# Performance work log

Hardware: AMD Instinct MI355X
Metric: run time of the kernel (lower is better)

Reference implementation:

```python
import jax, jax.numpy as jnp
import numpy as np
import math

BATCH, NODES, IN_DIM = 8, 2048, 64
HEADS, OUT_DIM = 4, 32
D = HEADS * OUT_DIM
N_NEIGHBORS = 32


def setup_inputs() -> dict:
    key = jax.random.key(0)
    ks = jax.random.split(key, 6)
    s = lambda fan: 1.0 / np.sqrt(fan)
    return {
        "x": jax.random.normal(ks[0], (BATCH, NODES, IN_DIM), jnp.float32),
        "Wq": jax.random.normal(ks[1], (D, IN_DIM), jnp.float32) * s(IN_DIM),
        "bq": jnp.zeros((D,), jnp.float32),
        "Wk": jax.random.normal(ks[2], (D, IN_DIM), jnp.float32) * s(IN_DIM),
        "bk": jnp.zeros((D,), jnp.float32),
        "mlp_w": jax.random.normal(ks[3], (HEADS, HEADS), jnp.float32) * s(HEADS),
        "mlp_b": jnp.zeros((HEADS,), jnp.float32),
        "ln_g": jnp.ones((NODES,), jnp.float32),
        "ln_b": jnp.zeros((NODES,), jnp.float32),
    }


def _layernorm(x, g, b, eps=1e-5):
    m = x.mean(-1, keepdims=True)
    v = x.var(-1, keepdims=True)
    return (x - m) * jax.lax.rsqrt(v + eps) * g + b


def _forward(x, Wq, bq, Wk, bk, mlp_w, mlp_b, ln_g, ln_b):
    B, N, _ = x.shape
    # static graph branch (computed in the original forward, but its result is
    # never used in the returned adjacency -- kept for fidelity; DCE'd under jit)
    adj_static = jax.nn.softmax(
        jax.nn.relu(_layernorm(jnp.einsum('bnc,bmc->bnm', x, x), ln_g, ln_b)), axis=1)
    del adj_static

    q = x @ Wq.T + bq  # (B,N,D)
    k = x @ Wk.T + bk
    # (B,D,N) -> (B,H,d,N)
    q = q.transpose(0, 2, 1).reshape(B, HEADS, OUT_DIM, N)
    k = k.transpose(0, 2, 1).reshape(B, HEADS, OUT_DIM, N)
    q = q.transpose(0, 1, 3, 2)  # (B,H,N,d)

    # torch.split(query, chunk, dim=-1) splits q over out_dim, k over nodes; zip
    # truncates to the shorter list -> only min(nq,nk) chunks are processed.
    chunk = math.ceil(N / 2)
    nq = math.ceil(OUT_DIM / chunk)
    nk = math.ceil(N / chunk)
    inv_sqrt_d = jnp.float32(1.0 / math.sqrt(OUT_DIM))
    outs = []
    for i in range(min(nq, nk)):
        qc = q[..., i * chunk:(i + 1) * chunk]          # (B,H,N,dc)
        kc = k[..., i * chunk:(i + 1) * chunk]          # (B,H,d,Uc)
        a = jnp.einsum('bhnd,bhdu->bhnu', qc, kc) * inv_sqrt_d
        # dropout is identity in eval mode; soft-threshold with beta=0
        a = jnp.sign(a) * jax.nn.relu(jnp.abs(a))
        # 1x1 conv over head channels + relu, residual add
        a = jax.nn.relu(jnp.einsum('oh,bhnu->bonu', mlp_w, a)
                        + mlp_b[None, :, None, None]) + a
        outs.append(a)
    attn = jnp.concatenate(outs, axis=-1)               # (B,H,N,U)

    scores = attn.sum(axis=1)                           # (B,N,U)
    vals, idx = jax.lax.top_k(scores, N_NEIGHBORS)      # sorted, largest
    adj = jnp.zeros((B, N, N), x.dtype)
    bi = jnp.arange(B)[:, None, None]
    ni = jnp.arange(N)[None, :, None]
    return adj.at[bi, ni, idx].add(vals)


def reference(x, Wq, bq, Wk, bk, mlp_w, mlp_b, ln_g, ln_b):
    return _forward(x, Wq, bq, Wk, bk, mlp_w, mlp_b, ln_g, ln_b)
```

## Files before the change

### kernel.cpp

```cpp
#include <hip/hip_runtime.h>
#include <cstdint>
#include <cstddef>

#define BATCH 8
#define NODES 2048
#define IN_DIM 64
#define DTOT 128
#define NKEY 1024
#define QGROUPS 128
#define KGROUPS 64
#define SROW 1028

typedef _Float16 half8v __attribute__((ext_vector_type(8)));
typedef float float4v __attribute__((ext_vector_type(4)));

__device__ __forceinline__ unsigned long long make_key(float v, int idx) {
    unsigned u = __float_as_uint(v);
    u = (u & 0x80000000u) ? ~u : (u | 0x80000000u);
    return ((unsigned long long)u << 32) | (unsigned)(1023 - idx);
}

__device__ __forceinline__ float key_val(unsigned hi) {
    return __uint_as_float((hi & 0x80000000u) ? (hi & 0x7fffffffu) : ~hi);
}

__global__ __launch_bounds__(256) void proj_qk(
    const float* __restrict__ x, const float* __restrict__ Wq, const float* __restrict__ bq,
    const float* __restrict__ Wk, const float* __restrict__ bk,
    _Float16* __restrict__ qfh, _Float16* __restrict__ qfl,
    _Float16* __restrict__ kfh, _Float16* __restrict__ kfl)
{
    __shared__ float xs[64 * 68];
    __shared__ float wsh[64 * 68];

    const int t = threadIdx.x;
    const int blk = blockIdx.x;
    const int b = blk / 96;
    const int idx = blk - b * 96;

    const float* W; const float* bias;
    _Float16* oh; _Float16* ol;
    int nbase, cbase; size_t gbase;
    if (idx < 64) {
        int nt = idx >> 1, ct = idx & 1;
        nbase = nt * 64; cbase = ct * 64;
        W = Wq; bias = bq; oh = qfh; ol = qfl;
        gbase = (size_t)b * QGROUPS + (nbase >> 4);
    } else {
        int i2 = idx - 64;
        int nt = i2 >> 1, ct = i2 & 1;
        nbase = nt * 64; cbase = ct * 64;
        W = Wk; bias = bk; oh = kfh; ol = kfl;
        gbase = (size_t)b * KGROUPS + (nbase >> 4);
    }
    const int hbase = cbase >> 5;

    #pragma unroll
    for (int rep = 0; rep < 4; ++rep) {
        int f = rep * 256 + t;
        int r = f >> 4, d4 = f & 15;
        float4 xv = *(const float4*)(x + ((size_t)(b * NODES + nbase + r)) * IN_DIM + d4 * 4);
        *(float4*)(xs + r * 68 + d4 * 4) = xv;
        float4 wv = *(const float4*)(W + (size_t)(cbase + r) * IN_DIM + d4 * 4);
        *(float4*)(wsh + r * 68 + d4 * 4) = wv;
    }
    __syncthreads();

    const int w = t >> 6, l = t & 63;
    const int n_sel = w * 4 + (l >> 4);
    const int ul = l & 15;

    float acc[4][4];
    #pragma unroll
    for (int i = 0; i < 4; ++i)
        #pragma unroll
        for (int j = 0; j < 4; ++j) acc[i][j] = 0.f;

    #pragma unroll
    for (int d4 = 0; d4 < 16; ++d4) {
        float4 xv[4], wv[4];
        #pragma unroll
        for (int i = 0; i < 4; ++i)
            xv[i] = *(const float4*)(xs + (n_sel * 4 + i) * 68 + d4 * 4);
        #pragma unroll
        for (int j = 0; j < 4; ++j)
            wv[j] = *(const float4*)(wsh + (j * 16 + ul) * 68 + d4 * 4);
        #pragma unroll
        for (int i = 0; i < 4; ++i)
            #pragma unroll
            for (int j = 0; j < 4; ++j)
                acc[i][j] += xv[i].x * wv[j].x + xv[i].y * wv[j].y +
                             xv[i].z * wv[j].z + xv[i].w * wv[j].w;
    }
    __syncthreads();

    #pragma unroll
    for (int j = 0; j < 4; ++j) {
        float bv = bias[cbase + j * 16 + ul];
        #pragma unroll
        for (int i = 0; i < 4; ++i)
            xs[(n_sel * 4 + i) * 68 + j * 16 + ul] = acc[i][j] + bv;
    }
    __syncthreads();

    #pragma unroll
    for (int rep = 0; rep < 2; ++rep) {
        int u = rep * 256 + t;
        int g = u >> 7, hh = (u >> 6) & 1, lf = u & 63;
        const float* src = xs + (g * 16 + (lf & 15)) * 68 + hh * 32 + (lf >> 4) * 8;
        float4 f0 = *(const float4*)src;
        float4 f1 = *(const float4*)(src + 4);
        float tmp[8] = {f0.x, f0.y, f0.z, f0.w, f1.x, f1.y, f1.z, f1.w};
        half8v hv, lv;
        #pragma unroll
        for (int e = 0; e < 8; ++e) {
            _Float16 hi = (_Float16)tmp[e];
            hv[e] = hi;
            lv[e] = (_Float16)(tmp[e] - (float)hi);
        }
        size_t dst = ((gbase + g) * 4 + hbase + hh) * (size_t)512 + lf * 8;
        *(half8v*)(oh + dst) = hv;
        *(half8v*)(ol + dst) = lv;
    }
}

__global__ __launch_bounds__(512, 4) void scores_topk(
    const _Float16* __restrict__ qfh, const _Float16* __restrict__ qfl,
    const _Float16* __restrict__ kfh, const _Float16* __restrict__ kfl,
    const float* __restrict__ mlpw, const float* __restrict__ mlpb,
    float* __restrict__ adj)
{
    __shared__ float sc[16 * SROW];
    __shared__ unsigned long long cand[8][64];

    const int t = threadIdx.x;
    const int blk = blockIdx.x;
    const int b = blk & 7;
    const int gq = blk >> 3;

    const int w = t >> 6, l = t & 63;
    const int quad = l >> 4, lane16 = l & 15;

    half8v Ah[4], Al[4];
    #pragma unroll
    for (int h = 0; h < 4; ++h) {
        size_t a = (((size_t)b * QGROUPS + gq) * 4 + h) * 512 + l * 8;
        Ah[h] = *(const half8v*)(qfh + a);
        Al[h] = *(const half8v*)(qfl + a);
    }

    float mw[4][4], mb4[4];
    #pragma unroll
    for (int o = 0; o < 4; ++o) {
        mb4[o] = mlpb[o];
        #pragma unroll
        for (int h = 0; h < 4; ++h) mw[o][h] = mlpw[o * 4 + h];
    }
    const float INV = 0.17677669529663687f;

    #pragma unroll 2
    for (int i = 0; i < 8; ++i) {
        const int g = w * 8 + i;
        float4v C[4];
        #pragma unroll
        for (int h = 0; h < 4; ++h) {
            size_t a = (((size_t)b * KGROUPS + g) * 4 + h) * 512 + l * 8;
            half8v Bh = *(const half8v*)(kfh + a);
            half8v Bl = *(const half8v*)(kfl + a);
            float4v c = {0.f, 0.f, 0.f, 0.f};
            c = __builtin_amdgcn_mfma_f32_16x16x32_f16(Ah[h], Bh, c, 0, 0, 0);
            c = __builtin_amdgcn_mfma_f32_16x16x32_f16(Ah[h], Bl, c, 0, 0, 0);
            c = __builtin_amdgcn_mfma_f32_16x16x32_f16(Al[h], Bh, c, 0, 0, 0);
            C[h] = c;
        }
        #pragma unroll
        for (int r = 0; r < 4; ++r) {
            float a0 = C[0][r] * INV, a1 = C[1][r] * INV;
            float a2 = C[2][r] * INV, a3 = C[3][r] * INV;
            float ssum = a0 + a1 + a2 + a3;
            #pragma unroll
            for (int o = 0; o < 4; ++o) {
                float to = mw[o][0] * a0 + mw[o][1] * a1 + mw[o][2] * a2 + mw[o][3] * a3 + mb4[o];
                ssum += fmaxf(to, 0.f);
            }
            sc[(quad * 4 + r) * SROW + g * 16 + lane16] = ssum;
        }
    }
    __syncthreads();

    for (int rr = 0; rr < 2; ++rr) {
        const int row = w * 2 + rr;
        float* R = sc + row * SROW;

        float4 vv[4];
        #pragma unroll
        for (int jj = 0; jj < 4; ++jj) vv[jj] = *(const float4*)(R + jj * 256 + l * 4);

        float m = vv[0].x;
        #pragma unroll
        for (int jj = 0; jj < 4; ++jj) {
            m = fmaxf(m, vv[jj].x); m = fmaxf(m, vv[jj].y);
            m = fmaxf(m, vv[jj].z); m = fmaxf(m, vv[jj].w);
        }

        unsigned km;
        { unsigned s = __float_as_uint(m); km = (s & 0x80000000u) ? ~s : (s | 0x80000000u); }
        unsigned accT = 0u;
        #pragma unroll
        for (int bit = 31; bit >= 0; --bit) {
            unsigned trial = accT | (1u << bit);
            if (__popcll(__ballot(km >= trial)) >= 32) accT = trial;
        }
        const float T = key_val(accT);

        cand[w][l] = 0ull;
        __builtin_amdgcn_wave_barrier();
        int total = 0;
        #pragma unroll
        for (int jj = 0; jj < 4; ++jj) {
            #pragma unroll
            for (int e = 0; e < 4; ++e) {
                float v = (e == 0) ? vv[jj].x : (e == 1) ? vv[jj].y : (e == 2) ? vv[jj].z : vv[jj].w;
                bool p = (v >= T);
                unsigned long long msk = __ballot(p);
                if (p) {
                    int pos = total + __popcll(msk & ((1ull << l) - 1ull));
                    if (pos < 64) cand[w][pos] = make_key(v, jj * 256 + l * 4 + e);
                }
                total += (int)__popcll(msk);
            }
        }
        __builtin_amdgcn_wave_barrier();

        bool win = false; float wval = 0.f; int widx = 0;
        if (total <= 64) {
            unsigned long long key = cand[w][l];
            unsigned hi = (unsigned)(key >> 32), lo = (unsigned)key;

            unsigned X = 0u;
            #pragma unroll
            for (int bit = 31; bit >= 0; --bit) {
                unsigned trial = X | (1u << bit);
                if (__popcll(__ballot(hi >= trial)) >= 32) X = trial;
            }
            int cgt = __popcll(__ballot(hi > X));
            int rem = 32 - cgt;
            unsigned Y = 0u;
            #pragma unroll
            for (int bit = 9; bit >= 0; --bit) {
                unsigned trial = Y | (1u << bit);
                if (__popcll(__ballot(hi == X && lo >= trial)) >= rem) Y = trial;
            }
            if (hi > X || (hi == X && lo >= Y)) {
                win = true;
                wval = key_val(hi);
                widx = 1023 - (int)lo;
            }
        } else {
            float vals[16];
            #pragma unroll
            for (int jj = 0; jj < 4; ++jj) {
                vals[jj * 4 + 0] = vv[jj].x; vals[jj * 4 + 1] = vv[jj].y;
                vals[jj * 4 + 2] = vv[jj].z; vals[jj * 4 + 3] = vv[jj].w;
            }
            float selv = 0.f; int seli = 0;
            #pragma unroll 1
            for (int it = 0; it < 32; ++it) {
                float bv = -3.4e38f; int bi = 0x7fffffff;
                #pragma unroll
                for (int s = 0; s < 16; ++s) {
                    int idx2 = (s >> 2) * 256 + l * 4 + (s & 3);
                    if (vals[s] > bv) { bv = vals[s]; bi = idx2; }
                }
                #pragma unroll
                for (int off = 1; off < 64; off <<= 1) {
                    float ov = __shfl_xor(bv, off, 64);
                    int oi = __shfl_xor(bi, off, 64);
                    if (ov > bv || (ov == bv && oi < bi)) { bv = ov; bi = oi; }
                }
                if (l == it) { selv = bv; seli = bi; }
                if (((bi >> 2) & 63) == l) {
                    int slot = ((bi >> 8) << 2) + (bi & 3);
                    #pragma unroll
                    for (int s = 0; s < 16; ++s) if (s == slot) vals[s] = -3.4e38f;
                }
            }
            if (l < 32) { win = true; wval = selv; widx = seli; }
        }

        __builtin_amdgcn_wave_barrier();
        #pragma unroll
        for (int jj = 0; jj < 16; ++jj) R[l + (jj << 6)] = 0.f;
        __builtin_amdgcn_wave_barrier();
        if (win) R[widx] = wval;
        __builtin_amdgcn_wave_barrier();

        float* rowptr = adj + ((size_t)(b * NODES + gq * 16 + row)) * NODES;
        #pragma unroll
        for (int jj = 0; jj < 8; ++jj) {
            int c4 = jj * 64 + l;
            float4 val;
            if (c4 < 256) val = *(const float4*)(R + c4 * 4);
            else          val = make_float4(0.f, 0.f, 0.f, 0.f);
            *(float4*)(rowptr + c4 * 4) = val;
        }
    }
}

extern "C" void kernel_launch(void* const* d_in, const int* in_sizes, int n_in,
                              void* d_out, int out_size, void* d_ws, size_t ws_size,
                              hipStream_t stream) {
    const float* x    = (const float*)d_in[0];
    const float* Wq   = (const float*)d_in[1];
    const float* bq   = (const float*)d_in[2];
    const float* Wk   = (const float*)d_in[3];
    const float* bk   = (const float*)d_in[4];
    const float* mlpw = (const float*)d_in[5];
    const float* mlpb = (const float*)d_in[6];

    _Float16* qfh = (_Float16*)d_ws;
    _Float16* qfl = qfh + (size_t)BATCH * NODES * DTOT;
    _Float16* kfh = qfl + (size_t)BATCH * NODES * DTOT;
    _Float16* kfl = kfh + (size_t)BATCH * NKEY * DTOT;
    float* adj = (float*)d_out;

    proj_qk<<<dim3(BATCH * 96), dim3(256), 0, stream>>>(x, Wq, bq, Wk, bk, qfh, qfl, kfh, kfl);
    scores_topk<<<dim3(BATCH * QGROUPS), dim3(512), 0, stream>>>(qfh, qfl, kfh, kfl, mlpw, mlpb, adj);
}
```

Before: 186.1 us.

## Split score tile into two 512-column passes to halve LDS and raise occupancy

The score/top-k kernel now computes 512 key columns at a time into a half-size shared buffer. Each pass selects its own top 32 candidates and stores them as packed keys. A final merge picks the global top 32 from the 64 candidates and writes the output row in two halves. Halving shared memory per block lets the launch bounds ask for 6 blocks per CU instead of 4, aiming to hide latency better. The cost is an extra selection pass, an extra block barrier, and more register pressure under the tighter launch bound.

```diff
diff --git a/kernel.cpp b/kernel.cpp
--- a/kernel.cpp
+++ b/kernel.cpp
@@ -9,15 +9,18 @@
 #define NKEY 1024
 #define QGROUPS 128
 #define KGROUPS 64
-#define SROW 1028
+#define SROW2 516
 
 typedef _Float16 half8v __attribute__((ext_vector_type(8)));
 typedef float float4v __attribute__((ext_vector_type(4)));
 
+__device__ __forceinline__ unsigned key_hi_u(float v) {
+    unsigned u = __float_as_uint(v);
+    return (u & 0x80000000u) ? ~u : (u | 0x80000000u);
+}
+
 __device__ __forceinline__ unsigned long long make_key(float v, int idx) {
-    unsigned u = __float_as_uint(v);
-    u = (u & 0x80000000u) ? ~u : (u | 0x80000000u);
-    return ((unsigned long long)u << 32) | (unsigned)(1023 - idx);
+    return ((unsigned long long)key_hi_u(v) << 32) | (unsigned)(1023 - idx);
 }
 
 __device__ __forceinline__ float key_val(unsigned hi) {
@@ -124,14 +127,103 @@
     }
 }
 
-__global__ __launch_bounds__(512, 4) void scores_topk(
+__device__ __forceinline__ void select_pass32(
+    const float* R, int ubase, int l,
+    unsigned long long* candw, unsigned long long* keyrow)
+{
+    float4 vv0 = *(const float4*)(R + l * 4);
+    float4 vv1 = *(const float4*)(R + 256 + l * 4);
+    float elems[8] = {vv0.x, vv0.y, vv0.z, vv0.w, vv1.x, vv1.y, vv1.z, vv1.w};
+
+    float m = elems[0];
+    #pragma unroll
+    for (int s = 1; s < 8; ++s) m = fmaxf(m, elems[s]);
+
+    unsigned km = key_hi_u(m);
+    unsigned accT = 0u;
+    #pragma unroll
+    for (int bit = 31; bit >= 0; --bit) {
+        unsigned trial = accT | (1u << bit);
+        if (__popcll(__ballot(km >= trial)) >= 32) accT = trial;
+    }
+    const float T = key_val(accT);
+
+    candw[l] = 0ull;
+    __builtin_amdgcn_wave_barrier();
+    int total = 0;
+    #pragma unroll
+    for (int s = 0; s < 8; ++s) {
+        float v = elems[s];
+        bool p = (v >= T);
+        unsigned long long msk = __ballot(p);
+        if (p) {
+            int pos = total + __popcll(msk & ((1ull << l) - 1ull));
+            if (pos < 64) candw[pos] = make_key(v, ubase + (s >> 2) * 256 + l * 4 + (s & 3));
+        }
+        total += (int)__popcll(msk);
+    }
+    __builtin_amdgcn_wave_barrier();
+
+    if (total <= 64) {
+        unsigned long long key = candw[l];
+        unsigned hi = (unsigned)(key >> 32), lo = (unsigned)key;
+        unsigned X = 0u;
+        #pragma unroll
+        for (int bit = 31; bit >= 0; --bit) {
+            unsigned trial = X | (1u << bit);
+            if (__popcll(__ballot(hi >= trial)) >= 32) X = trial;
+        }
+        int cgt = __popcll(__ballot(hi > X));
+        int rem = 32 - cgt;
+        unsigned Y = 0u;
+        #pragma unroll
+        for (int bit = 9; bit >= 0; --bit) {
+            unsigned trial = Y | (1u << bit);
+            if (__popcll(__ballot(hi == X && lo >= trial)) >= rem) Y = trial;
+        }
+        bool win = (hi > X) || (hi == X && lo >= Y);
+        unsigned long long wm = __ballot(win);
+        if (win) keyrow[__popcll(wm & ((1ull << l) - 1ull))] = key;
+    } else {
+        float vals[8];
+        #pragma unroll
+        for (int s = 0; s < 8; ++s) vals[s] = elems[s];
+        float selv = 0.f; int seli = 0;
+        #pragma unroll 1
+        for (int it = 0; it < 32; ++it) {
+            float bv = -3.4e38f; int bi = 0x7fffffff;
+            #pragma unroll
+            for (int s = 0; s < 8; ++s) {
+                int lu = (s >> 2) * 256 + l * 4 + (s & 3);
+                if (vals[s] > bv) { bv = vals[s]; bi = lu; }
+            }
+            #pragma unroll
+            for (int off = 1; off < 64; off <<= 1) {
+                float ov = __shfl_xor(bv, off, 64);
+                int oi = __shfl_xor(bi, off, 64);
+                if (ov > bv || (ov == bv && oi < bi)) { bv = ov; bi = oi; }
+            }
+            if (l == it) { selv = bv; seli = bi; }
+            if (((bi >> 2) & 63) == l) {
+                int slot = ((bi >> 8) << 2) + (bi & 3);
+                #pragma unroll
+                for (int s = 0; s < 8; ++s) if (s == slot) vals[s] = -3.4e38f;
+            }
+        }
+        if (l < 32) keyrow[l] = make_key(selv, ubase + seli);
+    }
+    __builtin_amdgcn_wave_barrier();
+}
+
+__global__ __launch_bounds__(512, 6) void scores_topk(
     const _Float16* __restrict__ qfh, const _Float16* __restrict__ qfl,
     const _Float16* __restrict__ kfh, const _Float16* __restrict__ kfl,
     const float* __restrict__ mlpw, const float* __restrict__ mlpb,
     float* __restrict__ adj)
 {
-    __shared__ float sc[16 * SROW];
+    __shared__ float sc[16 * SROW2];
     __shared__ unsigned long long cand[8][64];
+    __shared__ unsigned long long keys[16][64];
 
     const int t = threadIdx.x;
     const int blk = blockIdx.x;
@@ -158,152 +250,95 @@
     }
     const float INV = 0.17677669529663687f;
 
-    #pragma unroll 2
-    for (int i = 0; i < 8; ++i) {
-        const int g = w * 8 + i;
-        float4v C[4];
-        #pragma unroll
-        for (int h = 0; h < 4; ++h) {
-            size_t a = (((size_t)b * KGROUPS + g) * 4 + h) * 512 + l * 8;
-            half8v Bh = *(const half8v*)(kfh + a);
-            half8v Bl = *(const half8v*)(kfl + a);
-            float4v c = {0.f, 0.f, 0.f, 0.f};
-            c = __builtin_amdgcn_mfma_f32_16x16x32_f16(Ah[h], Bh, c, 0, 0, 0);
-            c = __builtin_amdgcn_mfma_f32_16x16x32_f16(Ah[h], Bl, c, 0, 0, 0);
-            c = __builtin_amdgcn_mfma_f32_16x16x32_f16(Al[h], Bh, c, 0, 0, 0);
-            C[h] = c;
-        }
-        #pragma unroll
-        for (int r = 0; r < 4; ++r) {
-            float a0 = C[0][r] * INV, a1 = C[1][r] * INV;
-            float a2 = C[2][r] * INV, a3 = C[3][r] * INV;
-            float ssum = a0 + a1 + a2 + a3;
-            #pragma unroll
-            for (int o = 0; o < 4; ++o) {
-                float to = mw[o][0] * a0 + mw[o][1] * a1 + mw[o][2] * a2 + mw[o][3] * a3 + mb4[o];
-                ssum += fmaxf(to, 0.f);
-            }
-            sc[(quad * 4 + r) * SROW + g * 16 + lane16] = ssum;
-        }
-    }
-    __syncthreads();
+    #pragma unroll 1
+    for (int pass = 0; pass < 2; ++pass) {
+        #pragma unroll 2
+        for (int i = 0; i < 4; ++i) {
+            const int g = pass * 32 + w * 4 + i;
+            float4v C[4];
+            #pragma unroll
+            for (int h = 0; h < 4; ++h) {
+                size_t a = (((size_t)b * KGROUPS + g) * 4 + h) * 512 + l * 8;
+                half8v Bh = *(const half8v*)(kfh + a);
+                half8v Bl = *(const half8v*)(kfl + a);
+                float4v c = {0.f, 0.f, 0.f, 0.f};
+                c = __builtin_amdgcn_mfma_f32_16x16x32_f16(Ah[h], Bh, c, 0, 0, 0);
+                c = __builtin_amdgcn_mfma_f32_16x16x32_f16(Ah[h], Bl, c, 0, 0, 0);
+                c = __builtin_amdgcn_mfma_f32_16x16x32_f16(Al[h], Bh, c, 0, 0, 0);
+                C[h] = c;
+            }
+            #pragma unroll
+            for (int r = 0; r < 4; ++r) {
+                float a0 = C[0][r] * INV, a1 = C[1][r] * INV;
+                float a2 = C[2][r] * INV, a3 = C[3][r] * INV;
+                float ssum = a0 + a1 + a2 + a3;
+                #pragma unroll
+                for (int o = 0; o < 4; ++o) {
+                    float to = mw[o][0] * a0 + mw[o][1] * a1 + mw[o][2] * a2 + mw[o][3] * a3 + mb4[o];
+                    ssum += fmaxf(to, 0.f);
+                }
+                sc[(quad * 4 + r) * SROW2 + (w * 4 + i) * 16 + lane16] = ssum;
+            }
+        }
+        __syncthreads();
+
+        for (int rr = 0; rr < 2; ++rr) {
+            const int row = w * 2 + rr;
+            select_pass32(sc + row * SROW2, pass * 512, l, cand[w], &keys[row][pass * 32]);
+        }
+        if (pass == 0) __syncthreads();
+    }
 
     for (int rr = 0; rr < 2; ++rr) {
         const int row = w * 2 + rr;
-        float* R = sc + row * SROW;
-
-        float4 vv[4];
-        #pragma unroll
-        for (int jj = 0; jj < 4; ++jj) vv[jj] = *(const float4*)(R + jj * 256 + l * 4);
-
-        float m = vv[0].x;
-        #pragma unroll
-        for (int jj = 0; jj < 4; ++jj) {
-            m = fmaxf(m, vv[jj].x); m = fmaxf(m, vv[jj].y);
-            m = fmaxf(m, vv[jj].z); m = fmaxf(m, vv[jj].w);
-        }
-
-        unsigned km;
-        { unsigned s = __float_as_uint(m); km = (s & 0x80000000u) ? ~s : (s | 0x80000000u); }
-        unsigned accT = 0u;
+        unsigned long long key = keys[row][l];
+        unsigned hi = (unsigned)(key >> 32), lo = (unsigned)key;
+
+        unsigned X = 0u;
         #pragma unroll
         for (int bit = 31; bit >= 0; --bit) {
-            unsigned trial = accT | (1u << bit);
-            if (__popcll(__ballot(km >= trial)) >= 32) accT = trial;
-        }
-        const float T = key_val(accT);
-
-        cand[w][l] = 0ull;
-        __builtin_amdgcn_wave_barrier();
-        int total = 0;
-        #pragma unroll
-        for (int jj = 0; jj < 4; ++jj) {
-            #pragma unroll
-            for (int e = 0; e < 4; ++e) {
-                float v = (e == 0) ? vv[jj].x : (e == 1) ? vv[jj].y : (e == 2) ? vv[jj].z : vv[jj].w;
-                bool p = (v >= T);
-                unsigned long long msk = __ballot(p);
-                if (p) {
-                    int pos = total + __popcll(msk & ((1ull << l) - 1ull));
-                    if (pos < 64) cand[w][pos] = make_key(v, jj * 256 + l * 4 + e);
-                }
-                total += (int)__popcll(msk);
-            }
-        }
-        __builtin_amdgcn_wave_barrier();
-
-        bool win = false; float wval = 0.f; int widx = 0;
-        if (total <= 64) {
-            unsigned long long key = cand[w][l];
-            unsigned hi = (unsigned)(key >> 32), lo = (unsigned)key;
-
-            unsigned X = 0u;
-            #pragma unroll
-            for (int bit = 31; bit >= 0; --bit) {
-                unsigned trial = X | (1u << bit);
-                if (__popcll(__ballot(hi >= trial)) >= 32) X = trial;
-            }
-            int cgt = __popcll(__ballot(hi > X));
-            int rem = 32 - cgt;
-            unsigned Y = 0u;
-            #pragma unroll
-            for (int bit = 9; bit >= 0; --bit) {
-                unsigned trial = Y | (1u << bit);
-                if (__popcll(__ballot(hi == X && lo >= trial)) >= rem) Y = trial;
-            }
-            if (hi > X || (hi == X && lo >= Y)) {
-                win = true;
-                wval = key_val(hi);
-                widx = 1023 - (int)lo;
-            }
-        } else {
-            float vals[16];
-            #pragma unroll
-            for (int jj = 0; jj < 4; ++jj) {
-                vals[jj * 4 + 0] = vv[jj].x; vals[jj * 4 + 1] = vv[jj].y;
-                vals[jj * 4 + 2] = vv[jj].z; vals[jj * 4 + 3] = vv[jj].w;
-            }
-            float selv = 0.f; int seli = 0;
-            #pragma unroll 1
-            for (int it = 0; it < 32; ++it) {
-                float bv = -3.4e38f; int bi = 0x7fffffff;
-                #pragma unroll
-                for (int s = 0; s < 16; ++s) {
-                    int idx2 = (s >> 2) * 256 + l * 4 + (s & 3);
-                    if (vals[s] > bv) { bv = vals[s]; bi = idx2; }
-                }
-                #pragma unroll
-                for (int off = 1; off < 64; off <<= 1) {
-                    float ov = __shfl_xor(bv, off, 64);
-                    int oi = __shfl_xor(bi, off, 64);
-                    if (ov > bv || (ov == bv && oi < bi)) { bv = ov; bi = oi; }
-                }
-                if (l == it) { selv = bv; seli = bi; }
-                if (((bi >> 2) & 63) == l) {
-                    int slot = ((bi >> 8) << 2) + (bi & 3);
-                    #pragma unroll
-                    for (int s = 0; s < 16; ++s) if (s == slot) vals[s] = -3.4e38f;
-                }
-            }
-            if (l < 32) { win = true; wval = selv; widx = seli; }
-        }
-
-        __builtin_amdgcn_wave_barrier();
-        #pragma unroll
-        for (int jj = 0; jj < 16; ++jj) R[l + (jj << 6)] = 0.f;
-        __builtin_amdgcn_wave_barrier();
-        if (win) R[widx] = wval;
-        __builtin_amdgcn_wave_barrier();
-
+            unsigned trial = X | (1u << bit);
+            if (__popcll(__ballot(hi >= trial)) >= 32) X = trial;
+        }
+        int cgt = __popcll(__ballot(hi > X));
+        int rem = 32 - cgt;
+        unsigned Y = 0u;
+        #pragma unroll
+        for (int bit = 9; bit >= 0; --bit) {
+            unsigned trial = Y | (1u << bit);
+            if (__popcll(__ballot(hi == X && lo >= trial)) >= rem) Y = trial;
+        }
+        const bool win = (hi > X) || (hi == X && lo >= Y);
+        const float wval = key_val(hi);
+        const int widx = 1023 - (int)lo;
+
+        float* R = sc + row * SROW2;
         float* rowptr = adj + ((size_t)(b * NODES + gq * 16 + row)) * NODES;
-        #pragma unroll
-        for (int jj = 0; jj < 8; ++jj) {
-            int c4 = jj * 64 + l;
-            float4 val;
-            if (c4 < 256) val = *(const float4*)(R + c4 * 4);
-            else          val = make_float4(0.f, 0.f, 0.f, 0.f);
-            *(float4*)(rowptr + c4 * 4) = val;
-        }
+        const float4 z4 = make_float4(0.f, 0.f, 0.f, 0.f);
+
+        __builtin_amdgcn_wave_barrier();
+        *(float4*)(R + l * 4) = z4;
+        *(float4*)(R + 256 + l * 4) = z4;
+        __builtin_amdgcn_wave_barrier();
+        if (win && widx < 512) R[widx] = wval;
+        __builtin_amdgcn_wave_barrier();
+        #pragma unroll
+        for (int jj = 0; jj < 2; ++jj)
+            *(float4*)(rowptr + jj * 256 + l * 4) = *(const float4*)(R + jj * 256 + l * 4);
+
+        __builtin_amdgcn_wave_barrier();
+        *(float4*)(R + l * 4) = z4;
+        *(float4*)(R + 256 + l * 4) = z4;
+        __builtin_amdgcn_wave_barrier();
+        if (win && widx >= 512) R[widx - 512] = wval;
+        __builtin_amdgcn_wave_barrier();
+        #pragma unroll
+        for (int jj = 0; jj < 2; ++jj)
+            *(float4*)(rowptr + 512 + jj * 256 + l * 4) = *(const float4*)(R + jj * 256 + l * 4);
+
+        #pragma unroll
+        for (int jj = 0; jj < 4; ++jj)
+            *(float4*)(rowptr + 1024 + jj * 256 + l * 4) = z4;
     }
 }
 
```

New measurement: 218.9 us. 17.6% more time.

## Split top-k selection from dense adjacency write into separate kernel

Applied to the files above, without the earlier changes.

The scores kernel now writes only the 32 selected values and indices per row to a workspace. A new lightweight kernel scatters them into a shared-memory row and streams the full 2048-wide dense adjacency row, zeros included, to global memory. The aim is to decouple the large output write, roughly 134 MB, from the compute-heavy scoring kernel so the write runs at full bandwidth with high occupancy. It adds an extra launch and a small round trip through global memory for the selected entries.

```diff
diff --git a/kernel.cpp b/kernel.cpp
--- a/kernel.cpp
+++ b/kernel.cpp
@@ -124,11 +124,11 @@
     }
 }
 
-__global__ __launch_bounds__(512, 4) void scores_topk(
+__global__ __launch_bounds__(512, 4) void scores_sel(
     const _Float16* __restrict__ qfh, const _Float16* __restrict__ qfl,
     const _Float16* __restrict__ kfh, const _Float16* __restrict__ kfl,
     const float* __restrict__ mlpw, const float* __restrict__ mlpb,
-    float* __restrict__ adj)
+    float* __restrict__ kval, int* __restrict__ kidx)
 {
     __shared__ float sc[16 * SROW];
     __shared__ unsigned long long cand[8][64];
@@ -190,7 +190,8 @@
 
     for (int rr = 0; rr < 2; ++rr) {
         const int row = w * 2 + rr;
-        float* R = sc + row * SROW;
+        const float* R = sc + row * SROW;
+        const size_t grow = (size_t)(b * NODES + gq * 16 + row);
 
         float4 vv[4];
         #pragma unroll
@@ -232,7 +233,6 @@
         }
         __builtin_amdgcn_wave_barrier();
 
-        bool win = false; float wval = 0.f; int widx = 0;
         if (total <= 64) {
             unsigned long long key = cand[w][l];
             unsigned hi = (unsigned)(key >> 32), lo = (unsigned)key;
@@ -251,10 +251,12 @@
                 unsigned trial = Y | (1u << bit);
                 if (__popcll(__ballot(hi == X && lo >= trial)) >= rem) Y = trial;
             }
-            if (hi > X || (hi == X && lo >= Y)) {
-                win = true;
-                wval = key_val(hi);
-                widx = 1023 - (int)lo;
+            const bool win = (hi > X) || (hi == X && lo >= Y);
+            unsigned long long wm = __ballot(win);
+            if (win) {
+                int pos = __popcll(wm & ((1ull << l) - 1ull));
+                kval[grow * 32 + pos] = key_val(hi);
+                kidx[grow * 32 + pos] = 1023 - (int)lo;
             }
         } else {
             float vals[16];
@@ -285,25 +287,41 @@
                     for (int s = 0; s < 16; ++s) if (s == slot) vals[s] = -3.4e38f;
                 }
             }
-            if (l < 32) { win = true; wval = selv; widx = seli; }
-        }
-
-        __builtin_amdgcn_wave_barrier();
-        #pragma unroll
-        for (int jj = 0; jj < 16; ++jj) R[l + (jj << 6)] = 0.f;
-        __builtin_amdgcn_wave_barrier();
-        if (win) R[widx] = wval;
-        __builtin_amdgcn_wave_barrier();
-
-        float* rowptr = adj + ((size_t)(b * NODES + gq * 16 + row)) * NODES;
-        #pragma unroll
-        for (int jj = 0; jj < 8; ++jj) {
-            int c4 = jj * 64 + l;
-            float4 val;
-            if (c4 < 256) val = *(const float4*)(R + c4 * 4);
-            else          val = make_float4(0.f, 0.f, 0.f, 0.f);
-            *(float4*)(rowptr + c4 * 4) = val;
-        }
+            if (l < 32) {
+                kval[grow * 32 + l] = selv;
+                kidx[grow * 32 + l] = seli;
+            }
+        }
+    }
+}
+
+__global__ __launch_bounds__(256) void write_adj(
+    const float* __restrict__ kval, const int* __restrict__ kidx,
+    float* __restrict__ adj)
+{
+    __shared__ float rowbuf[2 * 1024];
+
+    const int t = threadIdx.x;
+    const int row0 = blockIdx.x * 2;
+
+    #pragma unroll
+    for (int i = 0; i < 2; ++i)
+        *(float4*)(&rowbuf[(i * 256 + t) * 4]) = make_float4(0.f, 0.f, 0.f, 0.f);
+    __syncthreads();
+
+    if (t < 64) {
+        int r = t >> 5, j = t & 31;
+        size_t src = (size_t)(row0 + r) * 32 + j;
+        rowbuf[r * 1024 + kidx[src]] = kval[src];
+    }
+    __syncthreads();
+
+    const float4 z4 = make_float4(0.f, 0.f, 0.f, 0.f);
+    #pragma unroll
+    for (int r = 0; r < 2; ++r) {
+        float* rp = adj + (size_t)(row0 + r) * NODES;
+        *(float4*)(rp + t * 4) = *(const float4*)(&rowbuf[r * 1024 + t * 4]);
+        *(float4*)(rp + 1024 + t * 4) = z4;
     }
 }
 
@@ -322,8 +340,11 @@
     _Float16* qfl = qfh + (size_t)BATCH * NODES * DTOT;
     _Float16* kfh = qfl + (size_t)BATCH * NODES * DTOT;
     _Float16* kfl = kfh + (size_t)BATCH * NKEY * DTOT;
+    float* kval = (float*)(kfl + (size_t)BATCH * NKEY * DTOT);
+    int*   kidx = (int*)(kval + (size_t)BATCH * NODES * 32);
     float* adj = (float*)d_out;
 
     proj_qk<<<dim3(BATCH * 96), dim3(256), 0, stream>>>(x, Wq, bq, Wk, bk, qfh, qfl, kfh, kfl);
-    scores_topk<<<dim3(BATCH * QGROUPS), dim3(512), 0, stream>>>(qfh, qfl, kfh, kfl, mlpw, mlpb, adj);
-}
+    scores_sel<<<dim3(BATCH * QGROUPS), dim3(512), 0, stream>>>(qfh, qfl, kfh, kfl, mlpw, mlpb, kval, kidx);
+    write_adj<<<dim3(BATCH * NODES / 2), dim3(256), 0, stream>>>(kval, kidx, adj);
+}
```

New measurement: 202.9 us. 9.0% more time.
